# Kernel tuning notes

Hardware: AMD Instinct MI355X
Metric: run time of the kernel (lower is better)

The kernel has to match this reference:

```python
import jax, jax.numpy as jnp
import numpy as np

NX, NZ, NU, B = 16, 8, 4, 65536


def setup_inputs() -> dict:
    key = jax.random.key(0)
    ks = jax.random.split(key, 10)
    mu_prev = jax.random.normal(ks[0], (B, NX), dtype=jnp.float32)
    # PSD covariance per batch element: L L^T + 0.5 I
    L = 0.1 * jax.random.normal(ks[1], (B, NX, NX), dtype=jnp.float32)
    Sigma_prev = jnp.einsum('bij,bkj->bik', L, L) + 0.5 * jnp.eye(NX, dtype=jnp.float32)
    u = jax.random.normal(ks[2], (B, NU), dtype=jnp.float32)
    z = jax.random.normal(ks[3], (B, NZ), dtype=jnp.float32)
    # System matrices (shared across the batch); scaled to keep tanh unsaturated
    A = 0.1 * jax.random.normal(ks[4], (NX, NX), dtype=jnp.float32) + jnp.eye(NX, dtype=jnp.float32)
    Bm = 0.1 * jax.random.normal(ks[5], (NX, NU), dtype=jnp.float32)
    C = 0.2 * jax.random.normal(ks[6], (NZ, NX), dtype=jnp.float32)
    MQ = 0.1 * jax.random.normal(ks[7], (NZ, NZ), dtype=jnp.float32)
    Q = MQ @ MQ.T + 0.05 * jnp.eye(NZ, dtype=jnp.float32)   # measurement noise cov [nz,nz]
    MR = 0.1 * jax.random.normal(ks[8], (NX, NX), dtype=jnp.float32)
    R = MR @ MR.T + 0.01 * jnp.eye(NX, dtype=jnp.float32)   # process noise cov [nx,nx]
    return {'mu_prev': mu_prev, 'Sigma_prev': Sigma_prev, 'u': u, 'z': z,
            'A': A, 'Bm': Bm, 'C': C, 'Q': Q, 'R': R}


def reference(mu_prev, Sigma_prev, u, z, A, Bm, C, Q, R):
    # Discrete-time EKF propagate (already_discrete=True branch), batched via vmap.
    def f_sys(x, u):
        return jnp.tanh(A @ x + Bm @ u)

    def h_sys(x):
        return jnp.tanh(C @ x)

    I_nx = jnp.eye(NX, dtype=mu_prev.dtype)

    def step(mu, Sig, u_b, z_b):
        mu_bar = f_sys(mu, u_b)                      # [nx]
        G = jax.jacfwd(f_sys)(mu, u_b)               # [nx,nx] df/dx
        Sig_bar = R + G @ Sig @ G.T                  # [nx,nx]
        H = jax.jacfwd(h_sys)(mu_bar)                # [nz,nx] dh/dx
        tp = Sig_bar @ H.T                           # [nx,nz]
        K = tp @ jnp.linalg.inv(H @ tp + Q)          # [nx,nz] Kalman gain
        mu_now = mu_bar + K @ (z_b - h_sys(mu_bar))
        I_KH = I_nx - K @ H
        Sig_now = I_KH @ Sig_bar @ I_KH.T + K @ Q @ K.T  # Joseph form
        return mu_now, Sig_now

    return jax.vmap(step)(mu_prev, Sigma_prev, u, z)
```

## Files before the change

### kernel.cpp

```cpp
#include <hip/hip_runtime.h>
#include <math.h>


namespace {

constexpr int LPE    = 8;
constexpr int GROUPS = 32;
constexpr int TPB    = GROUPS * LPE;

constexpr int O_VT  = 0;
constexpr int O_TPT = 0;
constexpr int O_SI  = 128;
constexpr int O_MU  = 256;
constexpr int O_D   = 272;
constexpr int O_H   = 288;
constexpr int O_DH  = 296;
constexpr int GS    = 308;

__device__ __forceinline__ float dot4(float4 a, float4 b) {
  return a.x*b.x + a.y*b.y + a.z*b.z + a.w*b.w;
}

__device__ __forceinline__ float tanh_fast(float x) {
  float e = __expf(2.0f * x);
  return 1.0f - 2.0f * __builtin_amdgcn_rcpf(e + 1.0f);
}

#define SWZF(v, imm) __int_as_float(__builtin_amdgcn_ds_swizzle(__float_as_int(v), (imm)))

#define GJ_STEP(P)                                                         \
  {                                                                        \
    float ps[8], px[8];                                                    \
    _Pragma("unroll")                                                      \
    for (int j = 0; j < 8; j++) {                                          \
      if (j >= (P)) ps[j] = SWZF(s8[j], (((P) << 5) | 0x18));              \
      else          px[j] = SWZF(x8[j], (((P) << 5) | 0x18));              \
    }                                                                      \
    const float rp = __builtin_amdgcn_rcpf(ps[(P)]);                       \
    const float f  = (t == (P)) ? (ps[(P)] - 1.0f) : s8[(P)];              \
    _Pragma("unroll")                                                      \
    for (int j = 0; j < 8; j++) {                                          \
      if (j > (P))      s8[j] -= f * (ps[j] * rp);                         \
      else if (j < (P)) x8[j] -= f * (px[j] * rp);                         \
    }                                                                      \
    x8[(P)] -= f * rp;                                                     \
  }

__global__ __launch_bounds__(TPB)
void ekf_kernel(const float* __restrict__ mu_prev,
                const float* __restrict__ Sig_prev,
                const float* __restrict__ U,
                const float* __restrict__ Z,
                const float* __restrict__ A,
                const float* __restrict__ Bm,
                const float* __restrict__ C,
                const float* __restrict__ Q,
                const float* __restrict__ R,
                float* __restrict__ mu_out,
                float* __restrict__ sig_out,
                int Btot)
{
  __shared__ float lds[GS * GROUPS];
  const int tid = threadIdx.x;
  const int g = tid >> 3;
  const int t = tid & 7;
  int e = blockIdx.x * GROUPS + g;
  if (e >= Btot) e = Btot - 1;
  float* L = lds + g * GS;
  const int r0 = t, r1 = t + 8;

  float sig0[16], sig1[16];
  {
    const float4* s0 = (const float4*)(Sig_prev + (size_t)e * 256 + r0 * 16);
    const float4* s1 = (const float4*)(Sig_prev + (size_t)e * 256 + r1 * 16);
    #pragma unroll
    for (int c = 0; c < 4; c++) {
      float4 v0 = s0[c], v1 = s1[c];
      sig0[4*c+0]=v0.x; sig0[4*c+1]=v0.y; sig0[4*c+2]=v0.z; sig0[4*c+3]=v0.w;
      sig1[4*c+0]=v1.x; sig1[4*c+1]=v1.y; sig1[4*c+2]=v1.z; sig1[4*c+3]=v1.w;
    }
  }

  float mubar0, mubar1, d0loc, d1loc;
  {
    const float4* mr = (const float4*)(mu_prev + (size_t)e * 16);
    float4 m0 = mr[0], m1 = mr[1], m2 = mr[2], m3 = mr[3];
    const float4* a0 = (const float4*)(A + r0 * 16);
    const float4* a1 = (const float4*)(A + r1 * 16);
    float p0 = dot4(a0[0],m0)+dot4(a0[1],m1)+dot4(a0[2],m2)+dot4(a0[3],m3);
    float p1 = dot4(a1[0],m0)+dot4(a1[1],m1)+dot4(a1[2],m2)+dot4(a1[3],m3);
    float4 u4 = *(const float4*)(U + (size_t)e * 4);
    p0 += dot4(*(const float4*)(Bm + r0 * 4), u4);
    p1 += dot4(*(const float4*)(Bm + r1 * 4), u4);
    mubar0 = tanh_fast(p0); d0loc = 1.0f - mubar0 * mubar0;
    mubar1 = tanh_fast(p1); d1loc = 1.0f - mubar1 * mubar1;
  }
  L[O_MU + r0] = mubar0; L[O_MU + r1] = mubar1;
  L[O_D  + r0] = d0loc;  L[O_D  + r1] = d1loc;
  __builtin_amdgcn_wave_barrier();

  float4 ct0, ct1, ct2, ct3;
  float dhl;
  {
    const float4* cr = (const float4*)(C + t * 16);
    ct0 = cr[0]; ct1 = cr[1]; ct2 = cr[2]; ct3 = cr[3];
    const float4* mb = (const float4*)(L + O_MU);
    float ph = dot4(ct0,mb[0])+dot4(ct1,mb[1])+dot4(ct2,mb[2])+dot4(ct3,mb[3]);
    float hb = tanh_fast(ph); dhl = 1.0f - hb * hb;
    L[O_H + t] = hb; L[O_DH + t] = dhl;
  }
  __builtin_amdgcn_wave_barrier();
  float dh[8];
  {
    float4 v0 = *(const float4*)(L + O_DH);
    float4 v1 = *(const float4*)(L + O_DH + 4);
    dh[0]=v0.x; dh[1]=v0.y; dh[2]=v0.z; dh[3]=v0.w;
    dh[4]=v1.x; dh[5]=v1.y; dh[6]=v1.z; dh[7]=v1.w;
  }

  #pragma unroll
  for (int j = 0; j < 16; j++) {
    float acc0 = 0.f, acc1 = 0.f;
    #pragma unroll
    for (int k = 0; k < 16; k++) {
      float a = A[j*16 + k];
      acc0 += sig0[k] * a; acc1 += sig1[k] * a;
    }
    L[O_VT + j*16 + r0] = acc0;
    L[O_VT + j*16 + r1] = acc1;
  }
  __builtin_amdgcn_wave_barrier();

  float sb0[16], sb1[16];
  {
    float v0[16], v1[16];
    const float4* p0 = (const float4*)(L + O_VT + r0 * 16);
    const float4* p1 = (const float4*)(L + O_VT + r1 * 16);
    #pragma unroll
    for (int c = 0; c < 4; c++) {
      float4 x0 = p0[c], x1 = p1[c];
      v0[4*c+0]=x0.x; v0[4*c+1]=x0.y; v0[4*c+2]=x0.z; v0[4*c+3]=x0.w;
      v1[4*c+0]=x1.x; v1[4*c+1]=x1.y; v1[4*c+2]=x1.z; v1[4*c+3]=x1.w;
    }
    #pragma unroll
    for (int i = 0; i < 16; i++) {
      float acc0 = 0.f, acc1 = 0.f;
      #pragma unroll
      for (int k = 0; k < 16; k++) {
        float a = A[i*16 + k];
        acc0 += a * v0[k]; acc1 += a * v1[k];
      }
      sb0[i] = acc0; sb1[i] = acc1;
    }
  }
  __builtin_amdgcn_wave_barrier();

  {
    const float4* rr0 = (const float4*)(R + r0 * 16);
    const float4* rr1 = (const float4*)(R + r1 * 16);
    const float4* dv  = (const float4*)(L + O_D);
    #pragma unroll
    for (int c = 0; c < 4; c++) {
      float4 ra = rr0[c], rb = rr1[c], dd = dv[c];
      sb0[4*c+0] = ra.x + d0loc*sb0[4*c+0]*dd.x;
      sb0[4*c+1] = ra.y + d0loc*sb0[4*c+1]*dd.y;
      sb0[4*c+2] = ra.z + d0loc*sb0[4*c+2]*dd.z;
      sb0[4*c+3] = ra.w + d0loc*sb0[4*c+3]*dd.w;
      sb1[4*c+0] = rb.x + d1loc*sb1[4*c+0]*dd.x;
      sb1[4*c+1] = rb.y + d1loc*sb1[4*c+1]*dd.y;
      sb1[4*c+2] = rb.z + d1loc*sb1[4*c+2]*dd.z;
      sb1[4*c+3] = rb.w + d1loc*sb1[4*c+3]*dd.w;
    }
  }

  float tp0[8], tp1[8];
  #pragma unroll
  for (int m = 0; m < 8; m++) {
    float acc0 = 0.f, acc1 = 0.f;
    #pragma unroll
    for (int k = 0; k < 16; k++) {
      float c = C[m*16 + k];
      acc0 += sb0[k] * c; acc1 += sb1[k] * c;
    }
    tp0[m] = acc0 * dh[m]; tp1[m] = acc1 * dh[m];
    L[O_TPT + m*16 + r0] = tp0[m];
    L[O_TPT + m*16 + r1] = tp1[m];
  }
  __builtin_amdgcn_wave_barrier();

  float s8[8];
  {
    float4 q0 = *(const float4*)(Q + t * 8);
    float4 q1 = *(const float4*)(Q + t * 8 + 4);
    float qv[8] = {q0.x,q0.y,q0.z,q0.w,q1.x,q1.y,q1.z,q1.w};
    #pragma unroll
    for (int m = 0; m < 8; m++) {
      const float4* tr = (const float4*)(L + O_TPT + m * 16);
      float acc = dot4(ct0,tr[0]) + dot4(ct1,tr[1])
                + dot4(ct2,tr[2]) + dot4(ct3,tr[3]);
      s8[m] = acc * dhl + qv[m];
    }
  }

  float x8[8];
  #pragma unroll
  for (int j = 0; j < 8; j++) x8[j] = (j == t) ? 1.0f : 0.0f;
  GJ_STEP(0) GJ_STEP(1) GJ_STEP(2) GJ_STEP(3)
  GJ_STEP(4) GJ_STEP(5) GJ_STEP(6) GJ_STEP(7)

  *((float4*)(L + O_SI + t*8 + 0)) = make_float4(x8[0], x8[1], x8[2], x8[3]);
  *((float4*)(L + O_SI + t*8 + 4)) = make_float4(x8[4], x8[5], x8[6], x8[7]);
  __builtin_amdgcn_wave_barrier();

  float k0[8] = {0,0,0,0,0,0,0,0};
  float k1[8] = {0,0,0,0,0,0,0,0};
  #pragma unroll
  for (int m = 0; m < 8; m++) {
    float4 a = *(const float4*)(L + O_SI + m*8 + 0);
    float4 b = *(const float4*)(L + O_SI + m*8 + 4);
    float f0 = tp0[m], f1 = tp1[m];
    k0[0]+=f0*a.x; k0[1]+=f0*a.y; k0[2]+=f0*a.z; k0[3]+=f0*a.w;
    k0[4]+=f0*b.x; k0[5]+=f0*b.y; k0[6]+=f0*b.z; k0[7]+=f0*b.w;
    k1[0]+=f1*a.x; k1[1]+=f1*a.y; k1[2]+=f1*a.z; k1[3]+=f1*a.w;
    k1[4]+=f1*b.x; k1[5]+=f1*b.y; k1[6]+=f1*b.z; k1[7]+=f1*b.w;
  }

  {
    float4 z0 = *(const float4*)(Z + (size_t)e * 8);
    float4 z1 = *(const float4*)(Z + (size_t)e * 8 + 4);
    float4 h0 = *(const float4*)(L + O_H);
    float4 h1 = *(const float4*)(L + O_H + 4);
    float i0=z0.x-h0.x, i1=z0.y-h0.y, i2=z0.z-h0.z, i3=z0.w-h0.w;
    float i4=z1.x-h1.x, i5=z1.y-h1.y, i6=z1.z-h1.z, i7=z1.w-h1.w;
    float mu0 = mubar0 + k0[0]*i0+k0[1]*i1+k0[2]*i2+k0[3]*i3
                       + k0[4]*i4+k0[5]*i5+k0[6]*i6+k0[7]*i7;
    float mu1 = mubar1 + k1[0]*i0+k1[1]*i1+k1[2]*i2+k1[3]*i3
                       + k1[4]*i4+k1[5]*i5+k1[6]*i6+k1[7]*i7;
    mu_out[(size_t)e * 16 + r0] = mu0;
    mu_out[(size_t)e * 16 + r1] = mu1;
  }

  #pragma unroll
  for (int m = 0; m < 8; m++) {
    const float4* tr = (const float4*)(L + O_TPT + m * 16);
    float4 t0 = tr[0], t1 = tr[1], t2 = tr[2], t3 = tr[3];
    float km0 = k0[m], km1 = k1[m];
    sb0[0] -=km0*t0.x; sb0[1] -=km0*t0.y; sb0[2] -=km0*t0.z; sb0[3] -=km0*t0.w;
    sb0[4] -=km0*t1.x; sb0[5] -=km0*t1.y; sb0[6] -=km0*t1.z; sb0[7] -=km0*t1.w;
    sb0[8] -=km0*t2.x; sb0[9] -=km0*t2.y; sb0[10]-=km0*t2.z; sb0[11]-=km0*t2.w;
    sb0[12]-=km0*t3.x; sb0[13]-=km0*t3.y; sb0[14]-=km0*t3.z; sb0[15]-=km0*t3.w;
    sb1[0] -=km1*t0.x; sb1[1] -=km1*t0.y; sb1[2] -=km1*t0.z; sb1[3] -=km1*t0.w;
    sb1[4] -=km1*t1.x; sb1[5] -=km1*t1.y; sb1[6] -=km1*t1.z; sb1[7] -=km1*t1.w;
    sb1[8] -=km1*t2.x; sb1[9] -=km1*t2.y; sb1[10]-=km1*t2.z; sb1[11]-=km1*t2.w;
    sb1[12]-=km1*t3.x; sb1[13]-=km1*t3.y; sb1[14]-=km1*t3.z; sb1[15]-=km1*t3.w;
  }
  {
    float4* o0 = (float4*)(sig_out + (size_t)e * 256 + r0 * 16);
    float4* o1 = (float4*)(sig_out + (size_t)e * 256 + r1 * 16);
    o0[0] = make_float4(sb0[0],  sb0[1],  sb0[2],  sb0[3]);
    o0[1] = make_float4(sb0[4],  sb0[5],  sb0[6],  sb0[7]);
    o0[2] = make_float4(sb0[8],  sb0[9],  sb0[10], sb0[11]);
    o0[3] = make_float4(sb0[12], sb0[13], sb0[14], sb0[15]);
    o1[0] = make_float4(sb1[0],  sb1[1],  sb1[2],  sb1[3]);
    o1[1] = make_float4(sb1[4],  sb1[5],  sb1[6],  sb1[7]);
    o1[2] = make_float4(sb1[8],  sb1[9],  sb1[10], sb1[11]);
    o1[3] = make_float4(sb1[12], sb1[13], sb1[14], sb1[15]);
  }
}

}

extern "C" void kernel_launch(void* const* d_in, const int* in_sizes, int n_in,
                              void* d_out, int out_size, void* d_ws, size_t ws_size,
                              hipStream_t stream)
{
  const float* mu_prev = (const float*)d_in[0];
  const float* Sigma   = (const float*)d_in[1];
  const float* u       = (const float*)d_in[2];
  const float* z       = (const float*)d_in[3];
  const float* A       = (const float*)d_in[4];
  const float* Bm      = (const float*)d_in[5];
  const float* C       = (const float*)d_in[6];
  const float* Q       = (const float*)d_in[7];
  const float* R       = (const float*)d_in[8];

  const int Btot = in_sizes[0] / 16;
  float* mu_out  = (float*)d_out;
  float* sig_out = (float*)d_out + (size_t)Btot * 16;

  const int grid = (Btot + GROUPS - 1) / GROUPS;
  ekf_kernel<<<grid, TPB, 0, stream>>>(mu_prev, Sigma, u, z, A, Bm, C, Q, R,
                                       mu_out, sig_out, Btot);
}
```

Baseline: 159.7 us.

## Process two batch elements per 8-lane group to amortize matrix loads

Each 8-lane group now handles two EKF elements instead of one, halving the block size and keeping the per-group LDS layout but with separate A/B regions. Shared system-matrix reads (A, C, R, Q) and the Gauss-Jordan swizzle steps are interleaved across both elements, so each A/C load feeds twice the FMAs and independent instruction streams give more ILP. The cost is roughly double the live register arrays, which may lower occupancy or cause spills, and fewer waves in flight for hiding memory latency.

```diff
diff --git a/kernel.cpp b/kernel.cpp
--- a/kernel.cpp
+++ b/kernel.cpp
@@ -5,17 +5,17 @@
 namespace {
 
 constexpr int LPE    = 8;
-constexpr int GROUPS = 32;
+constexpr int GROUPS = 16;
 constexpr int TPB    = GROUPS * LPE;
 
-constexpr int O_VT  = 0;
-constexpr int O_TPT = 0;
-constexpr int O_SI  = 128;
-constexpr int O_MU  = 256;
-constexpr int O_D   = 272;
-constexpr int O_H   = 288;
-constexpr int O_DH  = 296;
-constexpr int GS    = 308;
+constexpr int O_VT    = 0;
+constexpr int O_TPT_A = 0;
+constexpr int O_TPT_B = 128;
+constexpr int O_SI_A  = 256;
+constexpr int O_SI_B  = 320;
+constexpr int O_MU_A  = 384, O_D_A = 400, O_H_A = 416, O_DH_A = 424;
+constexpr int O_MU_B  = 432, O_D_B = 448, O_H_B = 464, O_DH_B = 472;
+constexpr int GS      = 484;
 
 __device__ __forceinline__ float dot4(float4 a, float4 b) {
   return a.x*b.x + a.y*b.y + a.z*b.z + a.w*b.w;
@@ -28,22 +28,29 @@
 
 #define SWZF(v, imm) __int_as_float(__builtin_amdgcn_ds_swizzle(__float_as_int(v), (imm)))
 
-#define GJ_STEP(P)                                                         \
+#define GJ_STEP2(P)                                                        \
   {                                                                        \
-    float ps[8], px[8];                                                    \
+    float psA[8], pxA[8], psB[8], pxB[8];                                  \
     _Pragma("unroll")                                                      \
     for (int j = 0; j < 8; j++) {                                          \
-      if (j >= (P)) ps[j] = SWZF(s8[j], (((P) << 5) | 0x18));              \
-      else          px[j] = SWZF(x8[j], (((P) << 5) | 0x18));              \
+      if (j >= (P)) { psA[j] = SWZF(s8A[j], (((P) << 5) | 0x18));          \
+                      psB[j] = SWZF(s8B[j], (((P) << 5) | 0x18)); }        \
+      else          { pxA[j] = SWZF(x8A[j], (((P) << 5) | 0x18));          \
+                      pxB[j] = SWZF(x8B[j], (((P) << 5) | 0x18)); }        \
     }                                                                      \
-    const float rp = __builtin_amdgcn_rcpf(ps[(P)]);                       \
-    const float f  = (t == (P)) ? (ps[(P)] - 1.0f) : s8[(P)];              \
+    const float rpA = __builtin_amdgcn_rcpf(psA[(P)]);                     \
+    const float rpB = __builtin_amdgcn_rcpf(psB[(P)]);                     \
+    const float fA  = (t == (P)) ? (psA[(P)] - 1.0f) : s8A[(P)];           \
+    const float fB  = (t == (P)) ? (psB[(P)] - 1.0f) : s8B[(P)];           \
     _Pragma("unroll")                                                      \
     for (int j = 0; j < 8; j++) {                                          \
-      if (j > (P))      s8[j] -= f * (ps[j] * rp);                         \
-      else if (j < (P)) x8[j] -= f * (px[j] * rp);                         \
+      if (j > (P))      { s8A[j] -= fA * (psA[j] * rpA);                   \
+                          s8B[j] -= fB * (psB[j] * rpB); }                 \
+      else if (j < (P)) { x8A[j] -= fA * (pxA[j] * rpA);                   \
+                          x8B[j] -= fB * (pxB[j] * rpB); }                 \
     }                                                                      \
-    x8[(P)] -= f * rp;                                                     \
+    x8A[(P)] -= fA * rpA;                                                  \
+    x8B[(P)] -= fB * rpB;                                                  \
   }
 
 __global__ __launch_bounds__(TPB)
@@ -64,58 +71,86 @@
   const int tid = threadIdx.x;
   const int g = tid >> 3;
   const int t = tid & 7;
-  int e = blockIdx.x * GROUPS + g;
-  if (e >= Btot) e = Btot - 1;
+  int eA = blockIdx.x * (2 * GROUPS) + 2 * g;
+  int eB = eA + 1;
+  if (eA >= Btot) eA = Btot - 1;
+  if (eB >= Btot) eB = Btot - 1;
   float* L = lds + g * GS;
   const int r0 = t, r1 = t + 8;
 
-  float sig0[16], sig1[16];
-  {
-    const float4* s0 = (const float4*)(Sig_prev + (size_t)e * 256 + r0 * 16);
-    const float4* s1 = (const float4*)(Sig_prev + (size_t)e * 256 + r1 * 16);
+  float sA0[16], sA1[16], sB0[16], sB1[16];
+  {
+    const float4* a0 = (const float4*)(Sig_prev + (size_t)eA * 256 + r0 * 16);
+    const float4* a1 = (const float4*)(Sig_prev + (size_t)eA * 256 + r1 * 16);
+    const float4* b0 = (const float4*)(Sig_prev + (size_t)eB * 256 + r0 * 16);
+    const float4* b1 = (const float4*)(Sig_prev + (size_t)eB * 256 + r1 * 16);
     #pragma unroll
     for (int c = 0; c < 4; c++) {
-      float4 v0 = s0[c], v1 = s1[c];
-      sig0[4*c+0]=v0.x; sig0[4*c+1]=v0.y; sig0[4*c+2]=v0.z; sig0[4*c+3]=v0.w;
-      sig1[4*c+0]=v1.x; sig1[4*c+1]=v1.y; sig1[4*c+2]=v1.z; sig1[4*c+3]=v1.w;
-    }
-  }
-
-  float mubar0, mubar1, d0loc, d1loc;
-  {
-    const float4* mr = (const float4*)(mu_prev + (size_t)e * 16);
-    float4 m0 = mr[0], m1 = mr[1], m2 = mr[2], m3 = mr[3];
-    const float4* a0 = (const float4*)(A + r0 * 16);
-    const float4* a1 = (const float4*)(A + r1 * 16);
-    float p0 = dot4(a0[0],m0)+dot4(a0[1],m1)+dot4(a0[2],m2)+dot4(a0[3],m3);
-    float p1 = dot4(a1[0],m0)+dot4(a1[1],m1)+dot4(a1[2],m2)+dot4(a1[3],m3);
-    float4 u4 = *(const float4*)(U + (size_t)e * 4);
-    p0 += dot4(*(const float4*)(Bm + r0 * 4), u4);
-    p1 += dot4(*(const float4*)(Bm + r1 * 4), u4);
-    mubar0 = tanh_fast(p0); d0loc = 1.0f - mubar0 * mubar0;
-    mubar1 = tanh_fast(p1); d1loc = 1.0f - mubar1 * mubar1;
-  }
-  L[O_MU + r0] = mubar0; L[O_MU + r1] = mubar1;
-  L[O_D  + r0] = d0loc;  L[O_D  + r1] = d1loc;
+      float4 va0 = a0[c], va1 = a1[c], vb0 = b0[c], vb1 = b1[c];
+      sA0[4*c+0]=va0.x; sA0[4*c+1]=va0.y; sA0[4*c+2]=va0.z; sA0[4*c+3]=va0.w;
+      sA1[4*c+0]=va1.x; sA1[4*c+1]=va1.y; sA1[4*c+2]=va1.z; sA1[4*c+3]=va1.w;
+      sB0[4*c+0]=vb0.x; sB0[4*c+1]=vb0.y; sB0[4*c+2]=vb0.z; sB0[4*c+3]=vb0.w;
+      sB1[4*c+0]=vb1.x; sB1[4*c+1]=vb1.y; sB1[4*c+2]=vb1.z; sB1[4*c+3]=vb1.w;
+    }
+  }
+
+  float mubarA0, mubarA1, dA0, dA1, mubarB0, mubarB1, dB0, dB1;
+  {
+    const float4* ar0 = (const float4*)(A + r0 * 16);
+    const float4* ar1 = (const float4*)(A + r1 * 16);
+    float4 a00=ar0[0], a01=ar0[1], a02=ar0[2], a03=ar0[3];
+    float4 a10=ar1[0], a11=ar1[1], a12=ar1[2], a13=ar1[3];
+    float4 bm0 = *(const float4*)(Bm + r0 * 4);
+    float4 bm1 = *(const float4*)(Bm + r1 * 4);
+
+    const float4* mA = (const float4*)(mu_prev + (size_t)eA * 16);
+    float4 uA = *(const float4*)(U + (size_t)eA * 4);
+    float pA0 = dot4(a00,mA[0])+dot4(a01,mA[1])+dot4(a02,mA[2])+dot4(a03,mA[3])
+              + dot4(bm0,uA);
+    float pA1 = dot4(a10,mA[0])+dot4(a11,mA[1])+dot4(a12,mA[2])+dot4(a13,mA[3])
+              + dot4(bm1,uA);
+    const float4* mB = (const float4*)(mu_prev + (size_t)eB * 16);
+    float4 uB = *(const float4*)(U + (size_t)eB * 4);
+    float pB0 = dot4(a00,mB[0])+dot4(a01,mB[1])+dot4(a02,mB[2])+dot4(a03,mB[3])
+              + dot4(bm0,uB);
+    float pB1 = dot4(a10,mB[0])+dot4(a11,mB[1])+dot4(a12,mB[2])+dot4(a13,mB[3])
+              + dot4(bm1,uB);
+    mubarA0 = tanh_fast(pA0); dA0 = 1.0f - mubarA0*mubarA0;
+    mubarA1 = tanh_fast(pA1); dA1 = 1.0f - mubarA1*mubarA1;
+    mubarB0 = tanh_fast(pB0); dB0 = 1.0f - mubarB0*mubarB0;
+    mubarB1 = tanh_fast(pB1); dB1 = 1.0f - mubarB1*mubarB1;
+  }
+  L[O_MU_A + r0] = mubarA0; L[O_MU_A + r1] = mubarA1;
+  L[O_D_A  + r0] = dA0;     L[O_D_A  + r1] = dA1;
+  L[O_MU_B + r0] = mubarB0; L[O_MU_B + r1] = mubarB1;
+  L[O_D_B  + r0] = dB0;     L[O_D_B  + r1] = dB1;
   __builtin_amdgcn_wave_barrier();
 
   float4 ct0, ct1, ct2, ct3;
-  float dhl;
+  float dhlA, dhlB;
   {
     const float4* cr = (const float4*)(C + t * 16);
     ct0 = cr[0]; ct1 = cr[1]; ct2 = cr[2]; ct3 = cr[3];
-    const float4* mb = (const float4*)(L + O_MU);
-    float ph = dot4(ct0,mb[0])+dot4(ct1,mb[1])+dot4(ct2,mb[2])+dot4(ct3,mb[3]);
-    float hb = tanh_fast(ph); dhl = 1.0f - hb * hb;
-    L[O_H + t] = hb; L[O_DH + t] = dhl;
-  }
-  __builtin_amdgcn_wave_barrier();
-  float dh[8];
-  {
-    float4 v0 = *(const float4*)(L + O_DH);
-    float4 v1 = *(const float4*)(L + O_DH + 4);
-    dh[0]=v0.x; dh[1]=v0.y; dh[2]=v0.z; dh[3]=v0.w;
-    dh[4]=v1.x; dh[5]=v1.y; dh[6]=v1.z; dh[7]=v1.w;
+    const float4* ma = (const float4*)(L + O_MU_A);
+    const float4* mb = (const float4*)(L + O_MU_B);
+    float phA = dot4(ct0,ma[0])+dot4(ct1,ma[1])+dot4(ct2,ma[2])+dot4(ct3,ma[3]);
+    float phB = dot4(ct0,mb[0])+dot4(ct1,mb[1])+dot4(ct2,mb[2])+dot4(ct3,mb[3]);
+    float hbA = tanh_fast(phA); dhlA = 1.0f - hbA * hbA;
+    float hbB = tanh_fast(phB); dhlB = 1.0f - hbB * hbB;
+    L[O_H_A + t] = hbA; L[O_DH_A + t] = dhlA;
+    L[O_H_B + t] = hbB; L[O_DH_B + t] = dhlB;
+  }
+  __builtin_amdgcn_wave_barrier();
+  float dhA[8], dhB[8];
+  {
+    float4 a0 = *(const float4*)(L + O_DH_A);
+    float4 a1 = *(const float4*)(L + O_DH_A + 4);
+    float4 b0 = *(const float4*)(L + O_DH_B);
+    float4 b1 = *(const float4*)(L + O_DH_B + 4);
+    dhA[0]=a0.x; dhA[1]=a0.y; dhA[2]=a0.z; dhA[3]=a0.w;
+    dhA[4]=a1.x; dhA[5]=a1.y; dhA[6]=a1.z; dhA[7]=a1.w;
+    dhB[0]=b0.x; dhB[1]=b0.y; dhB[2]=b0.z; dhB[3]=b0.w;
+    dhB[4]=b1.x; dhB[5]=b1.y; dhB[6]=b1.z; dhB[7]=b1.w;
   }
 
   #pragma unroll
@@ -124,147 +159,234 @@
     #pragma unroll
     for (int k = 0; k < 16; k++) {
       float a = A[j*16 + k];
-      acc0 += sig0[k] * a; acc1 += sig1[k] * a;
+      acc0 += sA0[k] * a; acc1 += sA1[k] * a;
     }
     L[O_VT + j*16 + r0] = acc0;
     L[O_VT + j*16 + r1] = acc1;
   }
   __builtin_amdgcn_wave_barrier();
-
-  float sb0[16], sb1[16];
-  {
-    float v0[16], v1[16];
+  float vcA0[16], vcA1[16];
+  {
     const float4* p0 = (const float4*)(L + O_VT + r0 * 16);
     const float4* p1 = (const float4*)(L + O_VT + r1 * 16);
     #pragma unroll
     for (int c = 0; c < 4; c++) {
       float4 x0 = p0[c], x1 = p1[c];
-      v0[4*c+0]=x0.x; v0[4*c+1]=x0.y; v0[4*c+2]=x0.z; v0[4*c+3]=x0.w;
-      v1[4*c+0]=x1.x; v1[4*c+1]=x1.y; v1[4*c+2]=x1.z; v1[4*c+3]=x1.w;
-    }
-    #pragma unroll
-    for (int i = 0; i < 16; i++) {
-      float acc0 = 0.f, acc1 = 0.f;
-      #pragma unroll
-      for (int k = 0; k < 16; k++) {
-        float a = A[i*16 + k];
-        acc0 += a * v0[k]; acc1 += a * v1[k];
-      }
-      sb0[i] = acc0; sb1[i] = acc1;
-    }
-  }
-  __builtin_amdgcn_wave_barrier();
+      vcA0[4*c+0]=x0.x; vcA0[4*c+1]=x0.y; vcA0[4*c+2]=x0.z; vcA0[4*c+3]=x0.w;
+      vcA1[4*c+0]=x1.x; vcA1[4*c+1]=x1.y; vcA1[4*c+2]=x1.z; vcA1[4*c+3]=x1.w;
+    }
+  }
+  __builtin_amdgcn_wave_barrier();
+
+  #pragma unroll
+  for (int j = 0; j < 16; j++) {
+    float acc0 = 0.f, acc1 = 0.f;
+    #pragma unroll
+    for (int k = 0; k < 16; k++) {
+      float a = A[j*16 + k];
+      acc0 += sB0[k] * a; acc1 += sB1[k] * a;
+    }
+    L[O_VT + j*16 + r0] = acc0;
+    L[O_VT + j*16 + r1] = acc1;
+  }
+  __builtin_amdgcn_wave_barrier();
+  float vcB0[16], vcB1[16];
+  {
+    const float4* p0 = (const float4*)(L + O_VT + r0 * 16);
+    const float4* p1 = (const float4*)(L + O_VT + r1 * 16);
+    #pragma unroll
+    for (int c = 0; c < 4; c++) {
+      float4 x0 = p0[c], x1 = p1[c];
+      vcB0[4*c+0]=x0.x; vcB0[4*c+1]=x0.y; vcB0[4*c+2]=x0.z; vcB0[4*c+3]=x0.w;
+      vcB1[4*c+0]=x1.x; vcB1[4*c+1]=x1.y; vcB1[4*c+2]=x1.z; vcB1[4*c+3]=x1.w;
+    }
+  }
+  __builtin_amdgcn_wave_barrier();
+
+  float sbA0[16], sbA1[16], sbB0[16], sbB1[16];
+  #pragma unroll
+  for (int i = 0; i < 16; i++) {
+    float aA0 = 0.f, aA1 = 0.f, aB0 = 0.f, aB1 = 0.f;
+    #pragma unroll
+    for (int k = 0; k < 16; k++) {
+      float a = A[i*16 + k];
+      aA0 += a * vcA0[k]; aA1 += a * vcA1[k];
+      aB0 += a * vcB0[k]; aB1 += a * vcB1[k];
+    }
+    sbA0[i] = aA0; sbA1[i] = aA1; sbB0[i] = aB0; sbB1[i] = aB1;
+  }
 
   {
     const float4* rr0 = (const float4*)(R + r0 * 16);
     const float4* rr1 = (const float4*)(R + r1 * 16);
-    const float4* dv  = (const float4*)(L + O_D);
+    const float4* dvA = (const float4*)(L + O_D_A);
+    const float4* dvB = (const float4*)(L + O_D_B);
     #pragma unroll
     for (int c = 0; c < 4; c++) {
-      float4 ra = rr0[c], rb = rr1[c], dd = dv[c];
-      sb0[4*c+0] = ra.x + d0loc*sb0[4*c+0]*dd.x;
-      sb0[4*c+1] = ra.y + d0loc*sb0[4*c+1]*dd.y;
-      sb0[4*c+2] = ra.z + d0loc*sb0[4*c+2]*dd.z;
-      sb0[4*c+3] = ra.w + d0loc*sb0[4*c+3]*dd.w;
-      sb1[4*c+0] = rb.x + d1loc*sb1[4*c+0]*dd.x;
-      sb1[4*c+1] = rb.y + d1loc*sb1[4*c+1]*dd.y;
-      sb1[4*c+2] = rb.z + d1loc*sb1[4*c+2]*dd.z;
-      sb1[4*c+3] = rb.w + d1loc*sb1[4*c+3]*dd.w;
-    }
-  }
-
-  float tp0[8], tp1[8];
+      float4 ra = rr0[c], rb = rr1[c], da = dvA[c], db = dvB[c];
+      sbA0[4*c+0] = ra.x + dA0*sbA0[4*c+0]*da.x;
+      sbA0[4*c+1] = ra.y + dA0*sbA0[4*c+1]*da.y;
+      sbA0[4*c+2] = ra.z + dA0*sbA0[4*c+2]*da.z;
+      sbA0[4*c+3] = ra.w + dA0*sbA0[4*c+3]*da.w;
+      sbA1[4*c+0] = rb.x + dA1*sbA1[4*c+0]*da.x;
+      sbA1[4*c+1] = rb.y + dA1*sbA1[4*c+1]*da.y;
+      sbA1[4*c+2] = rb.z + dA1*sbA1[4*c+2]*da.z;
+      sbA1[4*c+3] = rb.w + dA1*sbA1[4*c+3]*da.w;
+      sbB0[4*c+0] = ra.x + dB0*sbB0[4*c+0]*db.x;
+      sbB0[4*c+1] = ra.y + dB0*sbB0[4*c+1]*db.y;
+      sbB0[4*c+2] = ra.z + dB0*sbB0[4*c+2]*db.z;
+      sbB0[4*c+3] = ra.w + dB0*sbB0[4*c+3]*db.w;
+      sbB1[4*c+0] = rb.x + dB1*sbB1[4*c+0]*db.x;
+      sbB1[4*c+1] = rb.y + dB1*sbB1[4*c+1]*db.y;
+      sbB1[4*c+2] = rb.z + dB1*sbB1[4*c+2]*db.z;
+      sbB1[4*c+3] = rb.w + dB1*sbB1[4*c+3]*db.w;
+    }
+  }
+
+  float tpA0[8], tpA1[8], tpB0[8], tpB1[8];
   #pragma unroll
   for (int m = 0; m < 8; m++) {
-    float acc0 = 0.f, acc1 = 0.f;
+    float aA0 = 0.f, aA1 = 0.f, aB0 = 0.f, aB1 = 0.f;
     #pragma unroll
     for (int k = 0; k < 16; k++) {
       float c = C[m*16 + k];
-      acc0 += sb0[k] * c; acc1 += sb1[k] * c;
-    }
-    tp0[m] = acc0 * dh[m]; tp1[m] = acc1 * dh[m];
-    L[O_TPT + m*16 + r0] = tp0[m];
-    L[O_TPT + m*16 + r1] = tp1[m];
-  }
-  __builtin_amdgcn_wave_barrier();
-
-  float s8[8];
+      aA0 += sbA0[k] * c; aA1 += sbA1[k] * c;
+      aB0 += sbB0[k] * c; aB1 += sbB1[k] * c;
+    }
+    tpA0[m] = aA0 * dhA[m]; tpA1[m] = aA1 * dhA[m];
+    tpB0[m] = aB0 * dhB[m]; tpB1[m] = aB1 * dhB[m];
+    L[O_TPT_A + m*16 + r0] = tpA0[m];
+    L[O_TPT_A + m*16 + r1] = tpA1[m];
+    L[O_TPT_B + m*16 + r0] = tpB0[m];
+    L[O_TPT_B + m*16 + r1] = tpB1[m];
+  }
+  __builtin_amdgcn_wave_barrier();
+
+  float s8A[8], s8B[8];
   {
     float4 q0 = *(const float4*)(Q + t * 8);
     float4 q1 = *(const float4*)(Q + t * 8 + 4);
     float qv[8] = {q0.x,q0.y,q0.z,q0.w,q1.x,q1.y,q1.z,q1.w};
     #pragma unroll
     for (int m = 0; m < 8; m++) {
-      const float4* tr = (const float4*)(L + O_TPT + m * 16);
-      float acc = dot4(ct0,tr[0]) + dot4(ct1,tr[1])
-                + dot4(ct2,tr[2]) + dot4(ct3,tr[3]);
-      s8[m] = acc * dhl + qv[m];
-    }
-  }
-
-  float x8[8];
-  #pragma unroll
-  for (int j = 0; j < 8; j++) x8[j] = (j == t) ? 1.0f : 0.0f;
-  GJ_STEP(0) GJ_STEP(1) GJ_STEP(2) GJ_STEP(3)
-  GJ_STEP(4) GJ_STEP(5) GJ_STEP(6) GJ_STEP(7)
-
-  *((float4*)(L + O_SI + t*8 + 0)) = make_float4(x8[0], x8[1], x8[2], x8[3]);
-  *((float4*)(L + O_SI + t*8 + 4)) = make_float4(x8[4], x8[5], x8[6], x8[7]);
-  __builtin_amdgcn_wave_barrier();
-
-  float k0[8] = {0,0,0,0,0,0,0,0};
-  float k1[8] = {0,0,0,0,0,0,0,0};
+      const float4* ta = (const float4*)(L + O_TPT_A + m * 16);
+      const float4* tb = (const float4*)(L + O_TPT_B + m * 16);
+      float accA = dot4(ct0,ta[0]) + dot4(ct1,ta[1])
+                 + dot4(ct2,ta[2]) + dot4(ct3,ta[3]);
+      float accB = dot4(ct0,tb[0]) + dot4(ct1,tb[1])
+                 + dot4(ct2,tb[2]) + dot4(ct3,tb[3]);
+      s8A[m] = accA * dhlA + qv[m];
+      s8B[m] = accB * dhlB + qv[m];
+    }
+  }
+
+  float x8A[8], x8B[8];
+  #pragma unroll
+  for (int j = 0; j < 8; j++) {
+    x8A[j] = (j == t) ? 1.0f : 0.0f;
+    x8B[j] = (j == t) ? 1.0f : 0.0f;
+  }
+  GJ_STEP2(0) GJ_STEP2(1) GJ_STEP2(2) GJ_STEP2(3)
+  GJ_STEP2(4) GJ_STEP2(5) GJ_STEP2(6) GJ_STEP2(7)
+
+  *((float4*)(L + O_SI_A + t*8 + 0)) = make_float4(x8A[0],x8A[1],x8A[2],x8A[3]);
+  *((float4*)(L + O_SI_A + t*8 + 4)) = make_float4(x8A[4],x8A[5],x8A[6],x8A[7]);
+  *((float4*)(L + O_SI_B + t*8 + 0)) = make_float4(x8B[0],x8B[1],x8B[2],x8B[3]);
+  *((float4*)(L + O_SI_B + t*8 + 4)) = make_float4(x8B[4],x8B[5],x8B[6],x8B[7]);
+  __builtin_amdgcn_wave_barrier();
+
+  float kA0[8]={0,0,0,0,0,0,0,0}, kA1[8]={0,0,0,0,0,0,0,0};
+  float kB0[8]={0,0,0,0,0,0,0,0}, kB1[8]={0,0,0,0,0,0,0,0};
   #pragma unroll
   for (int m = 0; m < 8; m++) {
-    float4 a = *(const float4*)(L + O_SI + m*8 + 0);
-    float4 b = *(const float4*)(L + O_SI + m*8 + 4);
-    float f0 = tp0[m], f1 = tp1[m];
-    k0[0]+=f0*a.x; k0[1]+=f0*a.y; k0[2]+=f0*a.z; k0[3]+=f0*a.w;
-    k0[4]+=f0*b.x; k0[5]+=f0*b.y; k0[6]+=f0*b.z; k0[7]+=f0*b.w;
-    k1[0]+=f1*a.x; k1[1]+=f1*a.y; k1[2]+=f1*a.z; k1[3]+=f1*a.w;
-    k1[4]+=f1*b.x; k1[5]+=f1*b.y; k1[6]+=f1*b.z; k1[7]+=f1*b.w;
-  }
-
-  {
-    float4 z0 = *(const float4*)(Z + (size_t)e * 8);
-    float4 z1 = *(const float4*)(Z + (size_t)e * 8 + 4);
-    float4 h0 = *(const float4*)(L + O_H);
-    float4 h1 = *(const float4*)(L + O_H + 4);
-    float i0=z0.x-h0.x, i1=z0.y-h0.y, i2=z0.z-h0.z, i3=z0.w-h0.w;
-    float i4=z1.x-h1.x, i5=z1.y-h1.y, i6=z1.z-h1.z, i7=z1.w-h1.w;
-    float mu0 = mubar0 + k0[0]*i0+k0[1]*i1+k0[2]*i2+k0[3]*i3
-                       + k0[4]*i4+k0[5]*i5+k0[6]*i6+k0[7]*i7;
-    float mu1 = mubar1 + k1[0]*i0+k1[1]*i1+k1[2]*i2+k1[3]*i3
-                       + k1[4]*i4+k1[5]*i5+k1[6]*i6+k1[7]*i7;
-    mu_out[(size_t)e * 16 + r0] = mu0;
-    mu_out[(size_t)e * 16 + r1] = mu1;
+    float4 aa = *(const float4*)(L + O_SI_A + m*8 + 0);
+    float4 ab = *(const float4*)(L + O_SI_A + m*8 + 4);
+    float4 ba = *(const float4*)(L + O_SI_B + m*8 + 0);
+    float4 bb = *(const float4*)(L + O_SI_B + m*8 + 4);
+    float fA0 = tpA0[m], fA1 = tpA1[m], fB0 = tpB0[m], fB1 = tpB1[m];
+    kA0[0]+=fA0*aa.x; kA0[1]+=fA0*aa.y; kA0[2]+=fA0*aa.z; kA0[3]+=fA0*aa.w;
+    kA0[4]+=fA0*ab.x; kA0[5]+=fA0*ab.y; kA0[6]+=fA0*ab.z; kA0[7]+=fA0*ab.w;
+    kA1[0]+=fA1*aa.x; kA1[1]+=fA1*aa.y; kA1[2]+=fA1*aa.z; kA1[3]+=fA1*aa.w;
+    kA1[4]+=fA1*ab.x; kA1[5]+=fA1*ab.y; kA1[6]+=fA1*ab.z; kA1[7]+=fA1*ab.w;
+    kB0[0]+=fB0*ba.x; kB0[1]+=fB0*ba.y; kB0[2]+=fB0*ba.z; kB0[3]+=fB0*ba.w;
+    kB0[4]+=fB0*bb.x; kB0[5]+=fB0*bb.y; kB0[6]+=fB0*bb.z; kB0[7]+=fB0*bb.w;
+    kB1[0]+=fB1*ba.x; kB1[1]+=fB1*ba.y; kB1[2]+=fB1*ba.z; kB1[3]+=fB1*ba.w;
+    kB1[4]+=fB1*bb.x; kB1[5]+=fB1*bb.y; kB1[6]+=fB1*bb.z; kB1[7]+=fB1*bb.w;
+  }
+
+  {
+    float4 za0 = *(const float4*)(Z + (size_t)eA * 8);
+    float4 za1 = *(const float4*)(Z + (size_t)eA * 8 + 4);
+    float4 ha0 = *(const float4*)(L + O_H_A);
+    float4 ha1 = *(const float4*)(L + O_H_A + 4);
+    float iA0=za0.x-ha0.x, iA1=za0.y-ha0.y, iA2=za0.z-ha0.z, iA3=za0.w-ha0.w;
+    float iA4=za1.x-ha1.x, iA5=za1.y-ha1.y, iA6=za1.z-ha1.z, iA7=za1.w-ha1.w;
+    float muA0 = mubarA0 + kA0[0]*iA0+kA0[1]*iA1+kA0[2]*iA2+kA0[3]*iA3
+                         + kA0[4]*iA4+kA0[5]*iA5+kA0[6]*iA6+kA0[7]*iA7;
+    float muA1 = mubarA1 + kA1[0]*iA0+kA1[1]*iA1+kA1[2]*iA2+kA1[3]*iA3
+                         + kA1[4]*iA4+kA1[5]*iA5+kA1[6]*iA6+kA1[7]*iA7;
+    mu_out[(size_t)eA * 16 + r0] = muA0;
+    mu_out[(size_t)eA * 16 + r1] = muA1;
+
+    float4 zb0 = *(const float4*)(Z + (size_t)eB * 8);
+    float4 zb1 = *(const float4*)(Z + (size_t)eB * 8 + 4);
+    float4 hb0 = *(const float4*)(L + O_H_B);
+    float4 hb1 = *(const float4*)(L + O_H_B + 4);
+    float iB0=zb0.x-hb0.x, iB1=zb0.y-hb0.y, iB2=zb0.z-hb0.z, iB3=zb0.w-hb0.w;
+    float iB4=zb1.x-hb1.x, iB5=zb1.y-hb1.y, iB6=zb1.z-hb1.z, iB7=zb1.w-hb1.w;
+    float muB0 = mubarB0 + kB0[0]*iB0+kB0[1]*iB1+kB0[2]*iB2+kB0[3]*iB3
+                         + kB0[4]*iB4+kB0[5]*iB5+kB0[6]*iB6+kB0[7]*iB7;
+    float muB1 = mubarB1 + kB1[0]*iB0+kB1[1]*iB1+kB1[2]*iB2+kB1[3]*iB3
+                         + kB1[4]*iB4+kB1[5]*iB5+kB1[6]*iB6+kB1[7]*iB7;
+    mu_out[(size_t)eB * 16 + r0] = muB0;
+    mu_out[(size_t)eB * 16 + r1] = muB1;
   }
 
   #pragma unroll
   for (int m = 0; m < 8; m++) {
-    const float4* tr = (const float4*)(L + O_TPT + m * 16);
-    float4 t0 = tr[0], t1 = tr[1], t2 = tr[2], t3 = tr[3];
-    float km0 = k0[m], km1 = k1[m];
-    sb0[0] -=km0*t0.x; sb0[1] -=km0*t0.y; sb0[2] -=km0*t0.z; sb0[3] -=km0*t0.w;
-    sb0[4] -=km0*t1.x; sb0[5] -=km0*t1.y; sb0[6] -=km0*t1.z; sb0[7] -=km0*t1.w;
-    sb0[8] -=km0*t2.x; sb0[9] -=km0*t2.y; sb0[10]-=km0*t2.z; sb0[11]-=km0*t2.w;
-    sb0[12]-=km0*t3.x; sb0[13]-=km0*t3.y; sb0[14]-=km0*t3.z; sb0[15]-=km0*t3.w;
-    sb1[0] -=km1*t0.x; sb1[1] -=km1*t0.y; sb1[2] -=km1*t0.z; sb1[3] -=km1*t0.w;
-    sb1[4] -=km1*t1.x; sb1[5] -=km1*t1.y; sb1[6] -=km1*t1.z; sb1[7] -=km1*t1.w;
-    sb1[8] -=km1*t2.x; sb1[9] -=km1*t2.y; sb1[10]-=km1*t2.z; sb1[11]-=km1*t2.w;
-    sb1[12]-=km1*t3.x; sb1[13]-=km1*t3.y; sb1[14]-=km1*t3.z; sb1[15]-=km1*t3.w;
-  }
-  {
-    float4* o0 = (float4*)(sig_out + (size_t)e * 256 + r0 * 16);
-    float4* o1 = (float4*)(sig_out + (size_t)e * 256 + r1 * 16);
-    o0[0] = make_float4(sb0[0],  sb0[1],  sb0[2],  sb0[3]);
-    o0[1] = make_float4(sb0[4],  sb0[5],  sb0[6],  sb0[7]);
-    o0[2] = make_float4(sb0[8],  sb0[9],  sb0[10], sb0[11]);
-    o0[3] = make_float4(sb0[12], sb0[13], sb0[14], sb0[15]);
-    o1[0] = make_float4(sb1[0],  sb1[1],  sb1[2],  sb1[3]);
-    o1[1] = make_float4(sb1[4],  sb1[5],  sb1[6],  sb1[7]);
-    o1[2] = make_float4(sb1[8],  sb1[9],  sb1[10], sb1[11]);
-    o1[3] = make_float4(sb1[12], sb1[13], sb1[14], sb1[15]);
+    const float4* ta = (const float4*)(L + O_TPT_A + m * 16);
+    const float4* tb = (const float4*)(L + O_TPT_B + m * 16);
+    float4 a0 = ta[0], a1 = ta[1], a2 = ta[2], a3 = ta[3];
+    float4 b0 = tb[0], b1 = tb[1], b2 = tb[2], b3 = tb[3];
+    float mA0 = kA0[m], mA1 = kA1[m], mB0 = kB0[m], mB1 = kB1[m];
+    sbA0[0] -=mA0*a0.x; sbA0[1] -=mA0*a0.y; sbA0[2] -=mA0*a0.z; sbA0[3] -=mA0*a0.w;
+    sbA0[4] -=mA0*a1.x; sbA0[5] -=mA0*a1.y; sbA0[6] -=mA0*a1.z; sbA0[7] -=mA0*a1.w;
+    sbA0[8] -=mA0*a2.x; sbA0[9] -=mA0*a2.y; sbA0[10]-=mA0*a2.z; sbA0[11]-=mA0*a2.w;
+    sbA0[12]-=mA0*a3.x; sbA0[13]-=mA0*a3.y; sbA0[14]-=mA0*a3.z; sbA0[15]-=mA0*a3.w;
+    sbA1[0] -=mA1*a0.x; sbA1[1] -=mA1*a0.y; sbA1[2] -=mA1*a0.z; sbA1[3] -=mA1*a0.w;
+    sbA1[4] -=mA1*a1.x; sbA1[5] -=mA1*a1.y; sbA1[6] -=mA1*a1.z; sbA1[7] -=mA1*a1.w;
+    sbA1[8] -=mA1*a2.x; sbA1[9] -=mA1*a2.y; sbA1[10]-=mA1*a2.z; sbA1[11]-=mA1*a2.w;
+    sbA1[12]-=mA1*a3.x; sbA1[13]-=mA1*a3.y; sbA1[14]-=mA1*a3.z; sbA1[15]-=mA1*a3.w;
+    sbB0[0] -=mB0*b0.x; sbB0[1] -=mB0*b0.y; sbB0[2] -=mB0*b0.z; sbB0[3] -=mB0*b0.w;
+    sbB0[4] -=mB0*b1.x; sbB0[5] -=mB0*b1.y; sbB0[6] -=mB0*b1.z; sbB0[7] -=mB0*b1.w;
+    sbB0[8] -=mB0*b2.x; sbB0[9] -=mB0*b2.y; sbB0[10]-=mB0*b2.z; sbB0[11]-=mB0*b2.w;
+    sbB0[12]-=mB0*b3.x; sbB0[13]-=mB0*b3.y; sbB0[14]-=mB0*b3.z; sbB0[15]-=mB0*b3.w;
+    sbB1[0] -=mB1*b0.x; sbB1[1] -=mB1*b0.y; sbB1[2] -=mB1*b0.z; sbB1[3] -=mB1*b0.w;
+    sbB1[4] -=mB1*b1.x; sbB1[5] -=mB1*b1.y; sbB1[6] -=mB1*b1.z; sbB1[7] -=mB1*b1.w;
+    sbB1[8] -=mB1*b2.x; sbB1[9] -=mB1*b2.y; sbB1[10]-=mB1*b2.z; sbB1[11]-=mB1*b2.w;
+    sbB1[12]-=mB1*b3.x; sbB1[13]-=mB1*b3.y; sbB1[14]-=mB1*b3.z; sbB1[15]-=mB1*b3.w;
+  }
+  {
+    float4* oA0 = (float4*)(sig_out + (size_t)eA * 256 + r0 * 16);
+    float4* oA1 = (float4*)(sig_out + (size_t)eA * 256 + r1 * 16);
+    oA0[0] = make_float4(sbA0[0],  sbA0[1],  sbA0[2],  sbA0[3]);
+    oA0[1] = make_float4(sbA0[4],  sbA0[5],  sbA0[6],  sbA0[7]);
+    oA0[2] = make_float4(sbA0[8],  sbA0[9],  sbA0[10], sbA0[11]);
+    oA0[3] = make_float4(sbA0[12], sbA0[13], sbA0[14], sbA0[15]);
+    oA1[0] = make_float4(sbA1[0],  sbA1[1],  sbA1[2],  sbA1[3]);
+    oA1[1] = make_float4(sbA1[4],  sbA1[5],  sbA1[6],  sbA1[7]);
+    oA1[2] = make_float4(sbA1[8],  sbA1[9],  sbA1[10], sbA1[11]);
+    oA1[3] = make_float4(sbA1[12], sbA1[13], sbA1[14], sbA1[15]);
+    float4* oB0 = (float4*)(sig_out + (size_t)eB * 256 + r0 * 16);
+    float4* oB1 = (float4*)(sig_out + (size_t)eB * 256 + r1 * 16);
+    oB0[0] = make_float4(sbB0[0],  sbB0[1],  sbB0[2],  sbB0[3]);
+    oB0[1] = make_float4(sbB0[4],  sbB0[5],  sbB0[6],  sbB0[7]);
+    oB0[2] = make_float4(sbB0[8],  sbB0[9],  sbB0[10], sbB0[11]);
+    oB0[3] = make_float4(sbB0[12], sbB0[13], sbB0[14], sbB0[15]);
+    oB1[0] = make_float4(sbB1[0],  sbB1[1],  sbB1[2],  sbB1[3]);
+    oB1[1] = make_float4(sbB1[4],  sbB1[5],  sbB1[6],  sbB1[7]);
+    oB1[2] = make_float4(sbB1[8],  sbB1[9],  sbB1[10], sbB1[11]);
+    oB1[3] = make_float4(sbB1[12], sbB1[13], sbB1[14], sbB1[15]);
   }
 }
 
@@ -288,7 +410,8 @@
   float* mu_out  = (float*)d_out;
   float* sig_out = (float*)d_out + (size_t)Btot * 16;
 
-  const int grid = (Btot + GROUPS - 1) / GROUPS;
+  const int EPB = 2 * GROUPS;
+  const int grid = (Btot + EPB - 1) / EPB;
   ekf_kernel<<<grid, TPB, 0, stream>>>(mu_prev, Sigma, u, z, A, Bm, C, Q, R,
                                        mu_out, sig_out, Btot);
 }
```

Result: slower. 172.4 us (+8.0%).

## Pack paired-row math into float2 vectors for packed FMA and halve block size

Applied to the files above, without the earlier changes.

Each thread's two covariance rows (r0, r1) now live in float2 vectors, so the compiler can emit packed FP32 FMAs (v_pk_fma_f32) for the A·Σ·Aᵀ, C products, gain and Joseph-update loops. The second A multiply is fused with the R + D·(…)·D scaling step. The S = H·tp dot product uses two packed lanes. Block size drops from 256 to 128 threads (16 groups), which changes the grid shape and LDS per block. The aim is to halve the VALU instruction count on the FP32 arithmetic; the risk is extra register pressure or repacking moves.

```diff
diff --git a/kernel.cpp b/kernel.cpp
--- a/kernel.cpp
+++ b/kernel.cpp
@@ -4,8 +4,14 @@
 
 namespace {
 
+typedef float v2f __attribute__((ext_vector_type(2)));
+
+__device__ __forceinline__ v2f mk2(float a, float b) {
+  v2f r; r.x = a; r.y = b; return r;
+}
+
 constexpr int LPE    = 8;
-constexpr int GROUPS = 32;
+constexpr int GROUPS = 16;
 constexpr int TPB    = GROUPS * LPE;
 
 constexpr int O_VT  = 0;
@@ -69,15 +75,17 @@
   float* L = lds + g * GS;
   const int r0 = t, r1 = t + 8;
 
-  float sig0[16], sig1[16];
+  v2f sigp[16];
   {
     const float4* s0 = (const float4*)(Sig_prev + (size_t)e * 256 + r0 * 16);
     const float4* s1 = (const float4*)(Sig_prev + (size_t)e * 256 + r1 * 16);
     #pragma unroll
     for (int c = 0; c < 4; c++) {
       float4 v0 = s0[c], v1 = s1[c];
-      sig0[4*c+0]=v0.x; sig0[4*c+1]=v0.y; sig0[4*c+2]=v0.z; sig0[4*c+3]=v0.w;
-      sig1[4*c+0]=v1.x; sig1[4*c+1]=v1.y; sig1[4*c+2]=v1.z; sig1[4*c+3]=v1.w;
+      sigp[4*c+0] = mk2(v0.x, v1.x);
+      sigp[4*c+1] = mk2(v0.y, v1.y);
+      sigp[4*c+2] = mk2(v0.z, v1.z);
+      sigp[4*c+3] = mk2(v0.w, v1.w);
     }
   }
 
@@ -118,73 +126,80 @@
     dh[4]=v1.x; dh[5]=v1.y; dh[6]=v1.z; dh[7]=v1.w;
   }
 
+  v2f vv[16];
   #pragma unroll
   for (int j = 0; j < 16; j++) {
-    float acc0 = 0.f, acc1 = 0.f;
+    v2f acc = {0.f, 0.f};
     #pragma unroll
     for (int k = 0; k < 16; k++) {
-      float a = A[j*16 + k];
-      acc0 += sig0[k] * a; acc1 += sig1[k] * a;
-    }
-    L[O_VT + j*16 + r0] = acc0;
-    L[O_VT + j*16 + r1] = acc1;
-  }
-  __builtin_amdgcn_wave_barrier();
-
-  float sb0[16], sb1[16];
-  {
-    float v0[16], v1[16];
+      const float a = A[j*16 + k];
+      acc += sigp[k] * a;
+    }
+    vv[j] = acc;
+  }
+  #pragma unroll
+  for (int j = 0; j < 16; j++) {
+    L[O_VT + j*16 + r0] = vv[j].x;
+    L[O_VT + j*16 + r1] = vv[j].y;
+  }
+  __builtin_amdgcn_wave_barrier();
+
+  v2f vcp[16];
+  {
     const float4* p0 = (const float4*)(L + O_VT + r0 * 16);
     const float4* p1 = (const float4*)(L + O_VT + r1 * 16);
     #pragma unroll
     for (int c = 0; c < 4; c++) {
       float4 x0 = p0[c], x1 = p1[c];
-      v0[4*c+0]=x0.x; v0[4*c+1]=x0.y; v0[4*c+2]=x0.z; v0[4*c+3]=x0.w;
-      v1[4*c+0]=x1.x; v1[4*c+1]=x1.y; v1[4*c+2]=x1.z; v1[4*c+3]=x1.w;
-    }
-    #pragma unroll
-    for (int i = 0; i < 16; i++) {
-      float acc0 = 0.f, acc1 = 0.f;
-      #pragma unroll
-      for (int k = 0; k < 16; k++) {
-        float a = A[i*16 + k];
-        acc0 += a * v0[k]; acc1 += a * v1[k];
-      }
-      sb0[i] = acc0; sb1[i] = acc1;
-    }
-  }
-  __builtin_amdgcn_wave_barrier();
-
+      vcp[4*c+0] = mk2(x0.x, x1.x);
+      vcp[4*c+1] = mk2(x0.y, x1.y);
+      vcp[4*c+2] = mk2(x0.z, x1.z);
+      vcp[4*c+3] = mk2(x0.w, x1.w);
+    }
+  }
+  __builtin_amdgcn_wave_barrier();
+
+  v2f sbp[16];
   {
     const float4* rr0 = (const float4*)(R + r0 * 16);
     const float4* rr1 = (const float4*)(R + r1 * 16);
     const float4* dv  = (const float4*)(L + O_D);
+    const v2f dpair = mk2(d0loc, d1loc);
     #pragma unroll
     for (int c = 0; c < 4; c++) {
       float4 ra = rr0[c], rb = rr1[c], dd = dv[c];
-      sb0[4*c+0] = ra.x + d0loc*sb0[4*c+0]*dd.x;
-      sb0[4*c+1] = ra.y + d0loc*sb0[4*c+1]*dd.y;
-      sb0[4*c+2] = ra.z + d0loc*sb0[4*c+2]*dd.z;
-      sb0[4*c+3] = ra.w + d0loc*sb0[4*c+3]*dd.w;
-      sb1[4*c+0] = rb.x + d1loc*sb1[4*c+0]*dd.x;
-      sb1[4*c+1] = rb.y + d1loc*sb1[4*c+1]*dd.y;
-      sb1[4*c+2] = rb.z + d1loc*sb1[4*c+2]*dd.z;
-      sb1[4*c+3] = rb.w + d1loc*sb1[4*c+3]*dd.w;
-    }
-  }
-
-  float tp0[8], tp1[8];
+      #pragma unroll
+      for (int q = 0; q < 4; q++) {
+        const int i = 4*c + q;
+        v2f acc = {0.f, 0.f};
+        #pragma unroll
+        for (int k = 0; k < 16; k++) {
+          const float a = A[i*16 + k];
+          acc += vcp[k] * a;
+        }
+        const float rx = (q==0)?ra.x:(q==1)?ra.y:(q==2)?ra.z:ra.w;
+        const float ry = (q==0)?rb.x:(q==1)?rb.y:(q==2)?rb.z:rb.w;
+        const float dq = (q==0)?dd.x:(q==1)?dd.y:(q==2)?dd.z:dd.w;
+        sbp[i] = mk2(rx, ry) + dpair * acc * dq;
+      }
+    }
+  }
+
+  v2f tpp[8];
   #pragma unroll
   for (int m = 0; m < 8; m++) {
-    float acc0 = 0.f, acc1 = 0.f;
+    v2f acc = {0.f, 0.f};
     #pragma unroll
     for (int k = 0; k < 16; k++) {
-      float c = C[m*16 + k];
-      acc0 += sb0[k] * c; acc1 += sb1[k] * c;
-    }
-    tp0[m] = acc0 * dh[m]; tp1[m] = acc1 * dh[m];
-    L[O_TPT + m*16 + r0] = tp0[m];
-    L[O_TPT + m*16 + r1] = tp1[m];
+      const float c = C[m*16 + k];
+      acc += sbp[k] * c;
+    }
+    tpp[m] = acc * dh[m];
+  }
+  #pragma unroll
+  for (int m = 0; m < 8; m++) {
+    L[O_TPT + m*16 + r0] = tpp[m].x;
+    L[O_TPT + m*16 + r1] = tpp[m].y;
   }
   __builtin_amdgcn_wave_barrier();
 
@@ -196,9 +211,17 @@
     #pragma unroll
     for (int m = 0; m < 8; m++) {
       const float4* tr = (const float4*)(L + O_TPT + m * 16);
-      float acc = dot4(ct0,tr[0]) + dot4(ct1,tr[1])
-                + dot4(ct2,tr[2]) + dot4(ct3,tr[3]);
-      s8[m] = acc * dhl + qv[m];
+      float4 t0 = tr[0], t1 = tr[1], t2 = tr[2], t3 = tr[3];
+      v2f acc = {0.f, 0.f};
+      acc += mk2(ct0.x, ct0.y) * mk2(t0.x, t0.y);
+      acc += mk2(ct0.z, ct0.w) * mk2(t0.z, t0.w);
+      acc += mk2(ct1.x, ct1.y) * mk2(t1.x, t1.y);
+      acc += mk2(ct1.z, ct1.w) * mk2(t1.z, t1.w);
+      acc += mk2(ct2.x, ct2.y) * mk2(t2.x, t2.y);
+      acc += mk2(ct2.z, ct2.w) * mk2(t2.z, t2.w);
+      acc += mk2(ct3.x, ct3.y) * mk2(t3.x, t3.y);
+      acc += mk2(ct3.z, ct3.w) * mk2(t3.z, t3.w);
+      s8[m] = (acc.x + acc.y) * dhl + qv[m];
     }
   }
 
@@ -212,17 +235,15 @@
   *((float4*)(L + O_SI + t*8 + 4)) = make_float4(x8[4], x8[5], x8[6], x8[7]);
   __builtin_amdgcn_wave_barrier();
 
-  float k0[8] = {0,0,0,0,0,0,0,0};
-  float k1[8] = {0,0,0,0,0,0,0,0};
+  v2f kp[8] = {{0.f,0.f},{0.f,0.f},{0.f,0.f},{0.f,0.f},
+               {0.f,0.f},{0.f,0.f},{0.f,0.f},{0.f,0.f}};
   #pragma unroll
   for (int m = 0; m < 8; m++) {
     float4 a = *(const float4*)(L + O_SI + m*8 + 0);
     float4 b = *(const float4*)(L + O_SI + m*8 + 4);
-    float f0 = tp0[m], f1 = tp1[m];
-    k0[0]+=f0*a.x; k0[1]+=f0*a.y; k0[2]+=f0*a.z; k0[3]+=f0*a.w;
-    k0[4]+=f0*b.x; k0[5]+=f0*b.y; k0[6]+=f0*b.z; k0[7]+=f0*b.w;
-    k1[0]+=f1*a.x; k1[1]+=f1*a.y; k1[2]+=f1*a.z; k1[3]+=f1*a.w;
-    k1[4]+=f1*b.x; k1[5]+=f1*b.y; k1[6]+=f1*b.z; k1[7]+=f1*b.w;
+    const v2f f = tpp[m];
+    kp[0] += f * a.x; kp[1] += f * a.y; kp[2] += f * a.z; kp[3] += f * a.w;
+    kp[4] += f * b.x; kp[5] += f * b.y; kp[6] += f * b.z; kp[7] += f * b.w;
   }
 
   {
@@ -232,39 +253,38 @@
     float4 h1 = *(const float4*)(L + O_H + 4);
     float i0=z0.x-h0.x, i1=z0.y-h0.y, i2=z0.z-h0.z, i3=z0.w-h0.w;
     float i4=z1.x-h1.x, i5=z1.y-h1.y, i6=z1.z-h1.z, i7=z1.w-h1.w;
-    float mu0 = mubar0 + k0[0]*i0+k0[1]*i1+k0[2]*i2+k0[3]*i3
-                       + k0[4]*i4+k0[5]*i5+k0[6]*i6+k0[7]*i7;
-    float mu1 = mubar1 + k1[0]*i0+k1[1]*i1+k1[2]*i2+k1[3]*i3
-                       + k1[4]*i4+k1[5]*i5+k1[6]*i6+k1[7]*i7;
-    mu_out[(size_t)e * 16 + r0] = mu0;
-    mu_out[(size_t)e * 16 + r1] = mu1;
+    v2f mup = mk2(mubar0, mubar1);
+    mup += kp[0]*i0; mup += kp[1]*i1; mup += kp[2]*i2; mup += kp[3]*i3;
+    mup += kp[4]*i4; mup += kp[5]*i5; mup += kp[6]*i6; mup += kp[7]*i7;
+    mu_out[(size_t)e * 16 + r0] = mup.x;
+    mu_out[(size_t)e * 16 + r1] = mup.y;
   }
 
   #pragma unroll
   for (int m = 0; m < 8; m++) {
     const float4* tr = (const float4*)(L + O_TPT + m * 16);
     float4 t0 = tr[0], t1 = tr[1], t2 = tr[2], t3 = tr[3];
-    float km0 = k0[m], km1 = k1[m];
-    sb0[0] -=km0*t0.x; sb0[1] -=km0*t0.y; sb0[2] -=km0*t0.z; sb0[3] -=km0*t0.w;
-    sb0[4] -=km0*t1.x; sb0[5] -=km0*t1.y; sb0[6] -=km0*t1.z; sb0[7] -=km0*t1.w;
-    sb0[8] -=km0*t2.x; sb0[9] -=km0*t2.y; sb0[10]-=km0*t2.z; sb0[11]-=km0*t2.w;
-    sb0[12]-=km0*t3.x; sb0[13]-=km0*t3.y; sb0[14]-=km0*t3.z; sb0[15]-=km0*t3.w;
-    sb1[0] -=km1*t0.x; sb1[1] -=km1*t0.y; sb1[2] -=km1*t0.z; sb1[3] -=km1*t0.w;
-    sb1[4] -=km1*t1.x; sb1[5] -=km1*t1.y; sb1[6] -=km1*t1.z; sb1[7] -=km1*t1.w;
-    sb1[8] -=km1*t2.x; sb1[9] -=km1*t2.y; sb1[10]-=km1*t2.z; sb1[11]-=km1*t2.w;
-    sb1[12]-=km1*t3.x; sb1[13]-=km1*t3.y; sb1[14]-=km1*t3.z; sb1[15]-=km1*t3.w;
+    const v2f km = kp[m];
+    sbp[0]  -= km * t0.x; sbp[1]  -= km * t0.y;
+    sbp[2]  -= km * t0.z; sbp[3]  -= km * t0.w;
+    sbp[4]  -= km * t1.x; sbp[5]  -= km * t1.y;
+    sbp[6]  -= km * t1.z; sbp[7]  -= km * t1.w;
+    sbp[8]  -= km * t2.x; sbp[9]  -= km * t2.y;
+    sbp[10] -= km * t2.z; sbp[11] -= km * t2.w;
+    sbp[12] -= km * t3.x; sbp[13] -= km * t3.y;
+    sbp[14] -= km * t3.z; sbp[15] -= km * t3.w;
   }
   {
     float4* o0 = (float4*)(sig_out + (size_t)e * 256 + r0 * 16);
     float4* o1 = (float4*)(sig_out + (size_t)e * 256 + r1 * 16);
-    o0[0] = make_float4(sb0[0],  sb0[1],  sb0[2],  sb0[3]);
-    o0[1] = make_float4(sb0[4],  sb0[5],  sb0[6],  sb0[7]);
-    o0[2] = make_float4(sb0[8],  sb0[9],  sb0[10], sb0[11]);
-    o0[3] = make_float4(sb0[12], sb0[13], sb0[14], sb0[15]);
-    o1[0] = make_float4(sb1[0],  sb1[1],  sb1[2],  sb1[3]);
-    o1[1] = make_float4(sb1[4],  sb1[5],  sb1[6],  sb1[7]);
-    o1[2] = make_float4(sb1[8],  sb1[9],  sb1[10], sb1[11]);
-    o1[3] = make_float4(sb1[12], sb1[13], sb1[14], sb1[15]);
+    o0[0] = make_float4(sbp[0].x,  sbp[1].x,  sbp[2].x,  sbp[3].x);
+    o0[1] = make_float4(sbp[4].x,  sbp[5].x,  sbp[6].x,  sbp[7].x);
+    o0[2] = make_float4(sbp[8].x,  sbp[9].x,  sbp[10].x, sbp[11].x);
+    o0[3] = make_float4(sbp[12].x, sbp[13].x, sbp[14].x, sbp[15].x);
+    o1[0] = make_float4(sbp[0].y,  sbp[1].y,  sbp[2].y,  sbp[3].y);
+    o1[1] = make_float4(sbp[4].y,  sbp[5].y,  sbp[6].y,  sbp[7].y);
+    o1[2] = make_float4(sbp[8].y,  sbp[9].y,  sbp[10].y, sbp[11].y);
+    o1[3] = make_float4(sbp[12].y, sbp[13].y, sbp[14].y, sbp[15].y);
   }
 }
 
```

Result: slower. 163.1 us (+2.2%).
